# Performance work log

Measured on AMD Instinct MI355X. Metric: run time of the kernel, lower is better.

The kernel has to match this reference:

```python
import jax, jax.numpy as jnp
import numpy as np

NUM_TRACKS = 64
WIN = 31


def setup_inputs() -> dict:
    key = jax.random.key(0)
    k1, k2 = jax.random.split(key)
    track_locs = jax.random.uniform(k1, (64, NUM_TRACKS * 2), dtype=jnp.float32)
    imgs = jax.random.uniform(k2, (64, 2, 512, 512, 1), dtype=jnp.float32)
    return {"track_locs": track_locs, "imgs": imgs}


def _conv_same(im, k):
    # im: [N, H, W, 1], k: [3, 3, 1, 1]
    return jax.lax.conv_general_dilated(
        im, k, (1, 1), 'SAME', dimension_numbers=('NHWC', 'HWIO', 'NHWC'))


def reference(track_locs, imgs):
    B, T, H, W, C = imgs.shape
    nt, win = NUM_TRACKS, WIN
    P = win * win
    scale = win / min(W, H)

    # sampling grid in [-1, 1], xy-indexed like tf.meshgrid default
    lin = jnp.linspace(-1.0, 1.0, win)
    x_t, y_t = jnp.meshgrid(lin, lin)
    grid = jnp.stack([x_t.reshape(P), y_t.reshape(P)])  # [2, P]

    locs = track_locs.reshape(B, nt, 2, 1) / scale       # [B, nt, 2, 1]
    samples = grid[None, None] + locs                    # [B, nt, 2, P]
    x = samples[:, :, 0] * (win * 0.5)                   # [B, nt, P]
    y = samples[:, :, 1] * (win * 0.5)
    x = jnp.broadcast_to(x[:, None], (B, 2, nt, P))      # tile over 2 frames
    y = jnp.broadcast_to(y[:, None], (B, 2, nt, P))

    x0 = jnp.clip(jnp.floor(x), 0, W - 1)
    x1 = jnp.clip(jnp.floor(x) + 1.0, 0, W - 1)
    y0 = jnp.clip(jnp.floor(y), 0, H - 1)
    y1 = jnp.clip(jnp.floor(y) + 1.0, 0, H - 1)

    wa = ((y1 - y) * (x1 - x))[..., None]
    wb = ((y1 - y) * (x - x0))[..., None]
    wc = ((y - y0) * (x1 - x))[..., None]
    wd = ((y - y0) * (x - x0))[..., None]

    x0i = x0.astype(jnp.int32); x1i = x1.astype(jnp.int32)
    y0i = y0.astype(jnp.int32); y1i = y1.astype(jnp.int32)

    frames = imgs[:, :2]                                  # [B, 2, H, W, C]
    bi = jnp.arange(B)[:, None, None, None]
    fi = jnp.arange(2)[None, :, None, None]
    Ia = frames[bi, fi, y0i, x0i]                         # [B, 2, nt, P, C]
    Ib = frames[bi, fi, y0i, x1i]
    Ic = frames[bi, fi, y1i, x0i]
    Id = frames[bi, fi, y1i, x1i]

    out = (wa * Ia + wb * Ib + wc * Ic + wd * Id).reshape(B, 2, nt, win, win, C)

    # Lucas-Kanade solve (computed as in original forward; return value is `out`)
    first_frame = out[:, 0]
    second_frame = out[:, 1]
    ff_comb = first_frame.reshape(B * nt, win, win, C)

    sobel_x = jnp.array([[-1., 0., 1.], [-2., 0., 2.], [-1., 0., 1.]],
                        jnp.float32).reshape(3, 3, 1, 1)
    sobel_y = jnp.array([[-1., -2., -1.], [0., 0., 0.], [1., 2., 1.]],
                        jnp.float32).reshape(3, 3, 1, 1)

    Ix = _conv_same(ff_comb, sobel_x).reshape(B, nt, win, win, C)
    Iy = _conv_same(ff_comb, sobel_y).reshape(B, nt, win, win, C)
    sum_Ix2 = jnp.sum(Ix * Ix, axis=(2, 3, 4))
    sum_Iy2 = jnp.sum(Iy * Iy, axis=(2, 3, 4))
    sum_IxIy = jnp.sum(Ix * Iy, axis=(2, 3, 4))
    ATA = jnp.stack([sum_Iy2, -sum_IxIy, -sum_IxIy, sum_Ix2], axis=-1).reshape(B, nt, 2, 2)
    ATA_det = (1.0 / (sum_Ix2 * sum_Iy2 - sum_IxIy * sum_IxIy)).reshape(B, nt, 1, 1)
    ATA_1 = ATA_det * ATA
    It = second_frame - first_frame
    sum_IxIt = jnp.sum(Ix * It, axis=(2, 3, 4))
    sum_IyIt = jnp.sum(Iy * It, axis=(2, 3, 4))
    b = jnp.stack([-sum_IxIt, -sum_IyIt], axis=-1).reshape(B, nt, 2, 1)
    VxVy = jnp.matmul(ATA_1, b)  # computed but unused, as in original
    del VxVy
    return out
```

## Files before the change

### kernel.cpp

```cpp
#include <hip/hip_runtime.h>
#include <hip/hip_bf16.h>

#define B_     64
#define NT_    64
#define WIN_   31
#define P_     (WIN_ * WIN_)
#define H_     512
#define W_     512


__global__ __launch_bounds__(256)
void motion_sample_kernel(const float* __restrict__ track_locs,
                          const float* __restrict__ imgs,
                          float* __restrict__ out) {
    const int blk = blockIdx.x;
    const int t = blk % NT_;
    const int f = (blk / NT_) & 1;
    const int b = blk / (NT_ * 2);

    const float scale = (float)WIN_ / (float)W_;
    const float tx = track_locs[b * (NT_ * 2) + 2 * t];
    const float ty = track_locs[b * (NT_ * 2) + 2 * t + 1];

    const float halfwin = (float)WIN_ * 0.5f;
    const float basex = (-1.0f + tx / scale) * halfwin;
    const float basey = (-1.0f + ty / scale) * halfwin;
    const float step  = (2.0f / (float)(WIN_ - 1)) * halfwin;

    const float* frame = imgs + (size_t)(b * 2 + f) * (H_ * W_);
    float* outp = out + (size_t)blk * P_;

    for (int p = threadIdx.x; p < P_; p += blockDim.x) {
        const int i = p / WIN_;
        const int j = p % WIN_;

        const float x = basex + (float)j * step;
        const float y = basey + (float)i * step;

        const float fx = floorf(x);
        const float fy = floorf(y);

        const float x0f = fminf(fmaxf(fx,        0.0f), (float)(W_ - 1));
        const float x1f = fminf(fmaxf(fx + 1.0f, 0.0f), (float)(W_ - 1));
        const float y0f = fminf(fmaxf(fy,        0.0f), (float)(H_ - 1));
        const float y1f = fminf(fmaxf(fy + 1.0f, 0.0f), (float)(H_ - 1));

        const float wa = (y1f - y) * (x1f - x);
        const float wb = (y1f - y) * (x - x0f);
        const float wc = (y - y0f) * (x1f - x);
        const float wd = (y - y0f) * (x - x0f);

        const int x0i = (int)x0f;
        const int x1i = (int)x1f;
        const int y0i = (int)y0f;
        const int y1i = (int)y1f;

        const float Ia = frame[y0i * W_ + x0i];
        const float Ib = frame[y0i * W_ + x1i];
        const float Ic = frame[y1i * W_ + x0i];
        const float Id = frame[y1i * W_ + x1i];

        outp[p] = wa * Ia + wb * Ib + wc * Ic + wd * Id;
    }
}

extern "C" void kernel_launch(void* const* d_in, const int* in_sizes, int n_in,
                              void* d_out, int out_size, void* d_ws, size_t ws_size,
                              hipStream_t stream) {
    const float* track_locs = (const float*)d_in[0];
    const float* imgs       = (const float*)d_in[1];
    float* out              = (float*)d_out;

    const int nblocks = B_ * 2 * NT_;
    motion_sample_kernel<<<nblocks, 256, 0, stream>>>(track_locs, imgs, out);
}
```

Measured before the change: 191.3 us.

## Stage patch windows in shared memory and process both frames per block

```diff
diff --git a/kernel.cpp b/kernel.cpp
--- a/kernel.cpp
+++ b/kernel.cpp
@@ -7,6 +7,8 @@
 #define P_     (WIN_ * WIN_)
 #define H_     512
 #define W_     512
+#define TW_    34
+#define TELEMS (TW_ * TW_)
 
 
 __global__ __launch_bounds__(256)
@@ -15,8 +17,7 @@
                           float* __restrict__ out) {
     const int blk = blockIdx.x;
     const int t = blk % NT_;
-    const int f = (blk / NT_) & 1;
-    const int b = blk / (NT_ * 2);
+    const int b = blk / NT_;
 
     const float scale = (float)WIN_ / (float)W_;
     const float tx = track_locs[b * (NT_ * 2) + 2 * t];
@@ -27,10 +28,30 @@
     const float basey = (-1.0f + ty / scale) * halfwin;
     const float step  = (2.0f / (float)(WIN_ - 1)) * halfwin;
 
-    const float* frame = imgs + (size_t)(b * 2 + f) * (H_ * W_);
-    float* outp = out + (size_t)blk * P_;
+    const int xstart = (int)floorf(basex);
+    const int ystart = (int)floorf(basey);
 
-    for (int p = threadIdx.x; p < P_; p += blockDim.x) {
+    __shared__ float tile0[TELEMS];
+    __shared__ float tile1[TELEMS];
+
+    const float* frame0 = imgs + (size_t)(b * 2 + 0) * (H_ * W_);
+    const float* frame1 = imgs + (size_t)(b * 2 + 1) * (H_ * W_);
+
+    for (int idx = threadIdx.x; idx < TELEMS; idx += 256) {
+        const int r = idx / TW_;
+        const int c = idx % TW_;
+        const int gy = min(max(ystart + r, 0), H_ - 1);
+        const int gx = min(max(xstart + c, 0), W_ - 1);
+        const int g = gy * W_ + gx;
+        tile0[idx] = frame0[g];
+        tile1[idx] = frame1[g];
+    }
+    __syncthreads();
+
+    float* out0 = out + (size_t)((b * 2 + 0) * NT_ + t) * P_;
+    float* out1 = out + (size_t)((b * 2 + 1) * NT_ + t) * P_;
+
+    for (int p = threadIdx.x; p < P_; p += 256) {
         const int i = p / WIN_;
         const int j = p % WIN_;
 
@@ -50,17 +71,21 @@
         const float wc = (y - y0f) * (x1f - x);
         const float wd = (y - y0f) * (x - x0f);
 
-        const int x0i = (int)x0f;
-        const int x1i = (int)x1f;
-        const int y0i = (int)y0f;
-        const int y1i = (int)y1f;
+        const int lx0 = (int)x0f - xstart;
+        const int lx1 = (int)x1f - xstart;
+        const int ly0 = (int)y0f - ystart;
+        const int ly1 = (int)y1f - ystart;
 
-        const float Ia = frame[y0i * W_ + x0i];
-        const float Ib = frame[y0i * W_ + x1i];
-        const float Ic = frame[y1i * W_ + x0i];
-        const float Id = frame[y1i * W_ + x1i];
+        const int a00 = ly0 * TW_ + lx0;
+        const int a01 = ly0 * TW_ + lx1;
+        const int a10 = ly1 * TW_ + lx0;
+        const int a11 = ly1 * TW_ + lx1;
 
-        outp[p] = wa * Ia + wb * Ib + wc * Ic + wd * Id;
+        const float r0 = wa * tile0[a00] + wb * tile0[a01] + wc * tile0[a10] + wd * tile0[a11];
+        const float r1 = wa * tile1[a00] + wb * tile1[a01] + wc * tile1[a10] + wd * tile1[a11];
+
+        out0[p] = r0;
+        out1[p] = r1;
     }
 }
 
@@ -71,6 +96,6 @@
     const float* imgs       = (const float*)d_in[1];
     float* out              = (float*)d_out;
 
-    const int nblocks = B_ * 2 * NT_;
+    const int nblocks = B_ * NT_;
     motion_sample_kernel<<<nblocks, 256, 0, stream>>>(track_locs, imgs, out);
 }
```

Measured after the change: 185.9 us. 1.03x faster.
